# Optimization experiments

Measured on AMD Instinct MI355X. Metric: run time of the kernel, lower is better.

## Reference

```python
import jax, jax.numpy as jnp
import numpy as np
import math

L = 24  # legendre_polys; output features = L*L = 576


def _sh_norm(l, m):
    # exact Python-int factorial ratio, then sqrt (same as original)
    return math.sqrt((2.0 * l + 1.0) * math.factorial(l - m) / (4 * math.pi * math.factorial(l + m)))


def setup_inputs() -> dict:
    key = jax.random.key(0)
    u = jax.random.uniform(key, (400000, 2), dtype=jnp.float32)
    ra = u[:, 0] * 360.0          # degrees [0, 360)
    dec = u[:, 1] * 180.0 - 90.0  # degrees [-90, 90)
    return {"ra_dec": jnp.stack([ra, dec], axis=1)}


def reference(ra_dec):
    ra, dec = ra_dec[:, 0], ra_dec[:, 1]
    phi = jnp.deg2rad(ra)
    theta = jnp.deg2rad(dec + 90.0)
    x = jnp.cos(theta)                      # [N]
    somx2 = jnp.sqrt((1.0 - x) * (1.0 + x))  # sin(theta) magnitude

    # Associated Legendre P_l^m(x) for all 0 <= m <= l < L via the SAME
    # recursion as the original (computed once per (l,m) instead of from
    # scratch each call -- identical math, O(L^2) total).
    P = {}
    pmm = jnp.ones_like(x)
    fact = 1.0
    for m in range(L):
        if m > 0:
            pmm = pmm * (-fact) * somx2  # P_m^m
            fact += 2.0
        P[(m, m)] = pmm
        if m + 1 < L:
            cur = x * (2.0 * m + 1.0) * pmm  # P_{m+1}^m
            P[(m + 1, m)] = cur
            prev = pmm
            for ll in range(m + 2, L):
                nxt = ((2.0 * ll - 1.0) * x * cur - (ll + m - 1.0) * prev) / (ll - m)
                P[(ll, m)] = nxt
                prev, cur = cur, nxt

    sqrt2 = math.sqrt(2.0)
    Y = []
    for l in range(L):
        for m in range(-l, l + 1):
            am = abs(m)
            K = _sh_norm(l, am)
            if m == 0:
                y = K * P[(l, 0)]
            elif m > 0:
                y = sqrt2 * K * jnp.cos(m * phi) * P[(l, m)]
            else:
                y = sqrt2 * K * jnp.sin(am * phi) * P[(l, am)]
            Y.append(y)
    return jnp.stack(Y, axis=-1)  # [N, L*L]
```

## Files before the change

### kernel.cpp

```cpp
#include <hip/hip_runtime.h>
#include <type_traits>

#define LMAX 24

typedef float f32x4 __attribute__((ext_vector_type(4)));

constexpr double csqrt_(double x) {
  double y = x > 1.0 ? x : 1.0;
  for (int i = 0; i < 300; ++i) y = 0.5 * (y + x / y);
  return y;
}
constexpr double cfact_(int n) {
  double r = 1.0;
  for (int i = 2; i <= n; ++i) r *= (double)i;
  return r;
}
constexpr double PI_ = 3.14159265358979323846;

struct KTab {
  float k[LMAX][LMAX];
  constexpr KTab() : k{} {
    for (int l = 0; l < LMAX; ++l)
      for (int m = 0; m <= l; ++m)
        k[l][m] = (float)csqrt_((2.0 * l + 1.0) * cfact_(l - m) /
                                (4.0 * PI_ * cfact_(l + m)));
  }
};
constexpr KTab KT{};
constexpr float SQRT2_ = 1.41421356237309504880f;

template <int N, int I = 0, typename F>
__device__ __forceinline__ void static_for(F&& f) {
  if constexpr (I < N) {
    f(std::integral_constant<int, I>{});
    static_for<N, I + 1>(f);
  }
}

#define CJ 32
#define STR 36

__global__ __launch_bounds__(256) void sh_kernel(const float* __restrict__ rd,
                                                 float* __restrict__ out, int n) {
  __shared__ float lds[4 * 64 * STR];

  const int tid = threadIdx.x;
  const int wave = tid >> 6;
  const int lane = tid & 63;
  const long long base_pt = (long long)blockIdx.x * 256 + wave * 64;
  const long long my_pt = base_pt + lane;
  const int src = my_pt < n ? (int)my_pt : 0;
  const bool full = (base_pt + 64) <= (long long)n;

  const float2 p = reinterpret_cast<const float2*>(rd)[src];
  const float D2R = 0.017453292519943295f;
  float phi = p.x * D2R;
  float theta = (p.y + 90.0f) * D2R;
  float x = cosf(theta);
  float somx2 = sqrtf((1.0f - x) * (1.0f + x));

  float cm[LMAX], sm[LMAX];
  cm[0] = 1.0f; sm[0] = 0.0f;
  float c1, s1;
  __sincosf(phi, &s1, &c1);
  cm[1] = c1; sm[1] = s1;
  float twoc = 2.0f * c1;
#pragma unroll
  for (int m = 2; m < LMAX; ++m) {
    cm[m] = twoc * cm[m - 1] - cm[m - 2];
    sm[m] = twoc * sm[m - 1] - sm[m - 2];
  }

  float cur[LMAX], prev[LMAX];
  float pmm = 1.0f;
  float buf[4];

  float* const wptr = lds + wave * (64 * STR) + lane * STR;
  const float* const rbase = lds + wave * (64 * STR);

  auto flush = [&](int jc) {
    __builtin_amdgcn_wave_barrier();
    if (full) {
#pragma unroll
      for (int t = 0; t < 8; ++t) {
        int pp = t * 8 + (lane >> 3);
        int off = pp * STR + (lane & 7) * 4;
        f32x4 v = *reinterpret_cast<const f32x4*>(rbase + off);
        __builtin_nontemporal_store(
            v, reinterpret_cast<f32x4*>(out + (base_pt + pp) * (size_t)(LMAX * LMAX) +
                                        jc * CJ + (lane & 7) * 4));
      }
    } else {
#pragma unroll
      for (int t = 0; t < 8; ++t) {
        int pp = t * 8 + (lane >> 3);
        int off = pp * STR + (lane & 7) * 4;
        f32x4 v = *reinterpret_cast<const f32x4*>(rbase + off);
        long long pt = base_pt + pp;
        if (pt < n) {
          __builtin_nontemporal_store(
              v, reinterpret_cast<f32x4*>(out + pt * (size_t)(LMAX * LMAX) +
                                          jc * CJ + (lane & 7) * 4));
        }
      }
    }
    __builtin_amdgcn_wave_barrier();
  };

  static_for<LMAX>([&](auto LC) {
    constexpr int l = decltype(LC)::value;

    static_for<l>([&](auto MC) {
      constexpr int m = decltype(MC)::value;
      constexpr float a = (float)(2 * l - 1);
      constexpr float b = (float)(l + m - 1);
      constexpr float inv = 1.0f / (float)(l - m);
      float nxt = (a * x * cur[m] - b * prev[m]) * inv;
      prev[m] = cur[m];
      cur[m] = nxt;
    });

    if constexpr (l > 0) {
      pmm = pmm * (-(float)(2 * l - 1)) * somx2;
    }
    cur[l] = pmm;
    prev[l] = 0.0f;

    static_for<2 * l + 1>([&](auto KC) {
      constexpr int m = decltype(KC)::value - l;
      constexpr int am = m < 0 ? -m : m;
      constexpr int j = l * l + l + m;
      constexpr float C = (m == 0) ? KT.k[l][0] : SQRT2_ * KT.k[l][am];
      float y;
      if constexpr (m == 0) {
        y = C * cur[0];
      } else if constexpr (m > 0) {
        y = C * (cm[am] * cur[am]);
      } else {
        y = C * (sm[am] * cur[am]);
      }
      buf[j & 3] = y;
      if constexpr ((j & 3) == 3) {
        *reinterpret_cast<f32x4*>(wptr + ((j & (CJ - 1)) & ~3)) =
            f32x4{buf[0], buf[1], buf[2], buf[3]};
      }
      if constexpr ((j & (CJ - 1)) == CJ - 1) {
        flush(j >> 5);
      }
    });
  });
}

extern "C" void kernel_launch(void* const* d_in, const int* in_sizes, int n_in,
                              void* d_out, int out_size, void* d_ws, size_t ws_size,
                              hipStream_t stream) {
  (void)n_in; (void)out_size; (void)d_ws; (void)ws_size;
  const float* rd = (const float*)d_in[0];
  float* out = (float*)d_out;
  int n = in_sizes[0] / 2;
  int grid = (n + 255) / 256;
  sh_kernel<<<grid, 256, 0, stream>>>(rd, out, n);
}
```

Baseline: 194.9 us.

## Use single-wave blocks, padded scalar LDS staging, and plain global stores

Shrinks each block to one 64-thread wave and changes the LDS row stride from 36 to 33. Results are now written to LDS one float at a time instead of packed into 4-wide vectors. Output stores drop the nontemporal hint and become ordinary stores, and `(2l-1)*x` is hoisted out of the Legendre recursion loop. The aim is fewer LDS bank conflicts and better block scheduling for this store-bound kernel. The catch is that with stride 33 the 16-byte LDS reads during flush are no longer 16-byte aligned, and losing the nontemporal hint changes how the large output stream interacts with the cache.

```diff
diff --git a/kernel.cpp b/kernel.cpp
--- a/kernel.cpp
+++ b/kernel.cpp
@@ -38,16 +38,14 @@
 }
 
 #define CJ 32
-#define STR 36
+#define STR 33
 
-__global__ __launch_bounds__(256) void sh_kernel(const float* __restrict__ rd,
-                                                 float* __restrict__ out, int n) {
-  __shared__ float lds[4 * 64 * STR];
+__global__ __launch_bounds__(64) void sh_kernel(const float* __restrict__ rd,
+                                                float* __restrict__ out, int n) {
+  __shared__ float lds[64 * STR];
 
-  const int tid = threadIdx.x;
-  const int wave = tid >> 6;
-  const int lane = tid & 63;
-  const long long base_pt = (long long)blockIdx.x * 256 + wave * 64;
+  const int lane = threadIdx.x;
+  const long long base_pt = (long long)blockIdx.x * 64;
   const long long my_pt = base_pt + lane;
   const int src = my_pt < n ? (int)my_pt : 0;
   const bool full = (base_pt + 64) <= (long long)n;
@@ -73,10 +71,9 @@
 
   float cur[LMAX], prev[LMAX];
   float pmm = 1.0f;
-  float buf[4];
 
-  float* const wptr = lds + wave * (64 * STR) + lane * STR;
-  const float* const rbase = lds + wave * (64 * STR);
+  float* const wptr = lds + lane * STR;
+  const float* const rbase = lds;
 
   auto flush = [&](int jc) {
     __builtin_amdgcn_wave_barrier();
@@ -86,9 +83,8 @@
         int pp = t * 8 + (lane >> 3);
         int off = pp * STR + (lane & 7) * 4;
         f32x4 v = *reinterpret_cast<const f32x4*>(rbase + off);
-        __builtin_nontemporal_store(
-            v, reinterpret_cast<f32x4*>(out + (base_pt + pp) * (size_t)(LMAX * LMAX) +
-                                        jc * CJ + (lane & 7) * 4));
+        *reinterpret_cast<f32x4*>(out + (base_pt + pp) * (size_t)(LMAX * LMAX) +
+                                  jc * CJ + (lane & 7) * 4) = v;
       }
     } else {
 #pragma unroll
@@ -98,9 +94,8 @@
         f32x4 v = *reinterpret_cast<const f32x4*>(rbase + off);
         long long pt = base_pt + pp;
         if (pt < n) {
-          __builtin_nontemporal_store(
-              v, reinterpret_cast<f32x4*>(out + pt * (size_t)(LMAX * LMAX) +
-                                          jc * CJ + (lane & 7) * 4));
+          *reinterpret_cast<f32x4*>(out + pt * (size_t)(LMAX * LMAX) +
+                                    jc * CJ + (lane & 7) * 4) = v;
         }
       }
     }
@@ -110,12 +105,12 @@
   static_for<LMAX>([&](auto LC) {
     constexpr int l = decltype(LC)::value;
 
+    const float ax = (float)(2 * l - 1) * x;
     static_for<l>([&](auto MC) {
       constexpr int m = decltype(MC)::value;
-      constexpr float a = (float)(2 * l - 1);
       constexpr float b = (float)(l + m - 1);
       constexpr float inv = 1.0f / (float)(l - m);
-      float nxt = (a * x * cur[m] - b * prev[m]) * inv;
+      float nxt = (ax * cur[m] - b * prev[m]) * inv;
       prev[m] = cur[m];
       cur[m] = nxt;
     });
@@ -139,11 +134,7 @@
       } else {
         y = C * (sm[am] * cur[am]);
       }
-      buf[j & 3] = y;
-      if constexpr ((j & 3) == 3) {
-        *reinterpret_cast<f32x4*>(wptr + ((j & (CJ - 1)) & ~3)) =
-            f32x4{buf[0], buf[1], buf[2], buf[3]};
-      }
+      wptr[j & (CJ - 1)] = y;
       if constexpr ((j & (CJ - 1)) == CJ - 1) {
         flush(j >> 5);
       }
@@ -158,6 +149,6 @@
   const float* rd = (const float*)d_in[0];
   float* out = (float*)d_out;
   int n = in_sizes[0] / 2;
-  int grid = (n + 255) / 256;
-  sh_kernel<<<grid, 256, 0, stream>>>(rd, out, n);
+  int grid = (n + 63) / 64;
+  sh_kernel<<<grid, 64, 0, stream>>>(rd, out, n);
 }
```

New measurement: 193.5 us. Within noise of the previous version (-0.7%).
